# Optimization experiments

Measured on AMD Instinct MI355X. Metric: run time of the kernel, lower is better.

The kernel has to match this reference:

```python
import jax, jax.numpy as jnp
import numpy as np

BATCH, IN_F, OUT_F, GRID_PLUS_ORDER = 8192, 1024, 1024, 8

def setup_inputs() -> dict:
    key = jax.random.key(0)
    k1, k2, k3 = jax.random.split(key, 3)
    x = jax.random.normal(k1, (BATCH, IN_F), dtype=jnp.float32)
    base_weight = jax.random.normal(k2, (OUT_F, IN_F), dtype=jnp.float32) * 0.03
    spline_weight = jax.random.normal(k3, (OUT_F, IN_F, GRID_PLUS_ORDER), dtype=jnp.float32) * 0.1
    return {"x": x, "base_weight": base_weight, "spline_weight": spline_weight}

def reference(x, base_weight, spline_weight):
    # base_output = F.linear(x, base_weight) -> x @ W_b^T
    base_output = x @ base_weight.T  # [B, out]
    # Original: sum_{i,g} silu(x)[b,i] * spline_weight[o,i,g]
    # The grid/order axis g is never contracted with x, so it collapses:
    # silu(x) @ spline_weight.sum(-1).T  -- identical math, no [O,B,I,G] blowup.
    w_spline = jnp.sum(spline_weight, axis=-1)  # [out, in]
    spline_output = jax.nn.silu(x) @ w_spline.T  # [B, out]
    return base_output + spline_output
```

## Files before the change

kernel.cpp:

```cpp
#include <hip/hip_runtime.h>
#include <hip/hip_bf16.h>


#define BATCH 8192
#define IN_F 1024
#define OUT_F 1024
#define KP 2048

typedef unsigned short ushort_t;
typedef __attribute__((ext_vector_type(8))) short short8;
typedef __attribute__((ext_vector_type(4))) float f32x4;

__device__ __forceinline__ ushort_t f2bf(float f) {
  union { float f; unsigned int u; } v;
  v.f = f;
  unsigned int u = v.u;
  u += 0x7fffu + ((u >> 16) & 1u);
  return (ushort_t)(u >> 16);
}

#define PREP_A_BLOCKS 4096
#define PREP_S_BLOCKS 1024
#define PREP_B_BLOCKS 1024
#define PREP_BLOCKS (PREP_A_BLOCKS + PREP_S_BLOCKS + PREP_B_BLOCKS)

__global__ __launch_bounds__(256) void prep_all(
    const float* __restrict__ x, const float* __restrict__ Wb,
    const float* __restrict__ Ws, ushort_t* __restrict__ Apack,
    ushort_t* __restrict__ Wpack) {
  const int blk = blockIdx.x;
  const int t = threadIdx.x;

  if (blk < PREP_A_BLOCKS) {
    const int idx = blk * 256 + t;
    const int b = idx >> 7;
    const int i = (idx & 127) << 3;
    const float4 x0 = *(const float4*)(x + ((size_t)b << 10) + i);
    const float4 x1 = *(const float4*)(x + ((size_t)b << 10) + i + 4);
    float xv[8] = {x0.x, x0.y, x0.z, x0.w, x1.x, x1.y, x1.z, x1.w};
    ushort_t vb[8], vs[8];
#pragma unroll
    for (int j = 0; j < 8; ++j) {
      vb[j] = f2bf(xv[j]);
      vs[j] = f2bf(xv[j] / (1.0f + __expf(-xv[j])));
    }
    ushort_t* row = Apack + ((size_t)b << 11);
    *(short8*)(row + i) = *(short8*)vb;
    *(short8*)(row + IN_F + i) = *(short8*)vs;
  } else if (blk < PREP_A_BLOCKS + PREP_S_BLOCKS) {
    const int idx = (blk - PREP_A_BLOCKS) * 256 + t;
    const int o = idx >> 8;
    const int i0 = (idx & 255) << 2;
    ushort_t vs[4];
#pragma unroll
    for (int j = 0; j < 4; ++j) {
      const float4* p = (const float4*)(Ws + ((((size_t)o << 10) + i0 + j) << 3));
      const float4 a = p[0];
      const float4 b = p[1];
      vs[j] = f2bf(((a.x + a.y) + (a.z + a.w)) + ((b.x + b.y) + (b.z + b.w)));
    }
    *(ushort4*)(Wpack + ((size_t)o << 11) + IN_F + i0) = *(ushort4*)vs;
  } else {
    const int idx = (blk - PREP_A_BLOCKS - PREP_S_BLOCKS) * 256 + t;
    const int o = idx >> 8;
    const int c = (idx & 255) << 2;
    const float4 w = *(const float4*)(Wb + ((size_t)o << 10) + c);
    ushort4 v;
    v.x = f2bf(w.x); v.y = f2bf(w.y); v.z = f2bf(w.z); v.w = f2bf(w.w);
    *(ushort4*)(Wpack + ((size_t)o << 11) + c) = v;
  }
}

__global__ __launch_bounds__(256) void gemm_packed(
    const ushort_t* __restrict__ A,
    const ushort_t* __restrict__ W,
    float* __restrict__ C) {
  __shared__ ushort_t As[2 * 4096];
  __shared__ ushort_t Bs[2 * 4096];

  const int t = threadIdx.x;
  const int flat = blockIdx.y * 8 + blockIdx.x;
  const int xcd = flat & 7;
  const int local = flat >> 3;
  const int nt = local >> 3;
  const int mt = xcd * 8 + (local & 7);

  const int lane = t & 63;
  const int wave = t >> 6;
  const int wr = wave >> 1;
  const int wc = wave & 1;

  const int r = t >> 2;
  const int c = t & 3;
  const ushort_t* a_g = A + ((size_t)(mt * 128 + r)) * KP + c * 8;
  const ushort_t* b_g = W + ((size_t)(nt * 128 + r)) * KP + c * 8;
  const size_t rowskip = (size_t)64 * KP;
  const int wbase = c * 1024 + ((r ^ (c << 2)) << 3);

  f32x4 acc[4][4];
#pragma unroll
  for (int mi = 0; mi < 4; ++mi)
#pragma unroll
    for (int ni = 0; ni < 4; ++ni) acc[mi][ni] = (f32x4){0.f, 0.f, 0.f, 0.f};

  const int ks = lane >> 4;
  const int ar = (wr * 64 + (lane & 15)) ^ (ks << 2);
  const int br = (wc * 64 + (lane & 15)) ^ (ks << 2);
  const int rbase = ks * 1024;

  {
    uint4 la0 = *(const uint4*)(a_g);
    uint4 la1 = *(const uint4*)(a_g + rowskip);
    uint4 lb0 = *(const uint4*)(b_g);
    uint4 lb1 = *(const uint4*)(b_g + rowskip);
    *(uint4*)(As + wbase) = la0;
    *(uint4*)(As + wbase + 512) = la1;
    *(uint4*)(Bs + wbase) = lb0;
    *(uint4*)(Bs + wbase + 512) = lb1;
  }
  __syncthreads();

  int poff = 0;
  for (int k0 = 0; k0 < KP; k0 += 32) {
    const bool more = (k0 + 32) < KP;
    uint4 na0, na1, nb0, nb1;
    if (more) {
      na0 = *(const uint4*)(a_g + k0 + 32);
      na1 = *(const uint4*)(a_g + k0 + 32 + rowskip);
      nb0 = *(const uint4*)(b_g + k0 + 32);
      nb1 = *(const uint4*)(b_g + k0 + 32 + rowskip);
    }

    const ushort_t* ab = As + poff + rbase;
    const ushort_t* bb = Bs + poff + rbase;
    short8 af[4], bfr[4];
#pragma unroll
    for (int mi = 0; mi < 4; ++mi)
      af[mi] = *(const short8*)(ab + ((ar + mi * 16) << 3));
#pragma unroll
    for (int ni = 0; ni < 4; ++ni)
      bfr[ni] = *(const short8*)(bb + ((br + ni * 16) << 3));

#pragma unroll
    for (int mi = 0; mi < 4; ++mi)
#pragma unroll
      for (int ni = 0; ni < 4; ++ni)
        acc[mi][ni] = __builtin_amdgcn_mfma_f32_16x16x32_bf16(af[mi], bfr[ni], acc[mi][ni], 0, 0, 0);

    if (more) {
      const int qoff = poff ^ 4096;
      *(uint4*)(As + qoff + wbase) = na0;
      *(uint4*)(As + qoff + wbase + 512) = na1;
      *(uint4*)(Bs + qoff + wbase) = nb0;
      *(uint4*)(Bs + qoff + wbase + 512) = nb1;
      __syncthreads();
    }
    poff ^= 4096;
  }

  const int col0 = nt * 128 + wc * 64 + (lane & 15);
  const int row0 = mt * 128 + wr * 64 + ((lane >> 4) << 2);
#pragma unroll
  for (int mi = 0; mi < 4; ++mi)
#pragma unroll
    for (int ni = 0; ni < 4; ++ni) {
      float* cp = C + (size_t)(row0 + mi * 16) * OUT_F + col0 + ni * 16;
#pragma unroll
      for (int rr = 0; rr < 4; ++rr) cp[(size_t)rr * OUT_F] = acc[mi][ni][rr];
    }
}

extern "C" void kernel_launch(void* const* d_in, const int* in_sizes, int n_in,
                              void* d_out, int out_size, void* d_ws, size_t ws_size,
                              hipStream_t stream) {
  const float* x = (const float*)d_in[0];
  const float* wb = (const float*)d_in[1];
  const float* ws = (const float*)d_in[2];
  float* out = (float*)d_out;

  ushort_t* Apack = (ushort_t*)d_ws;
  ushort_t* Wpack = (ushort_t*)((char*)d_ws + (size_t)BATCH * KP * 2);

  prep_all<<<PREP_BLOCKS, 256, 0, stream>>>(x, wb, ws, Apack, Wpack);
  gemm_packed<<<dim3(OUT_F / 128, BATCH / 128), 256, 0, stream>>>(Apack, Wpack, out);
}
```

Measured before the change: 153.7 us.

## Restructure GEMM with 256x128 tiles, async global-to-LDS loads, triple buffering

Result: faster. 143.6 us (-6.5%).

```diff
diff --git a/kernel.cpp b/kernel.cpp
--- a/kernel.cpp
+++ b/kernel.cpp
@@ -71,31 +71,92 @@
   }
 }
 
-__global__ __launch_bounds__(256) void gemm_packed(
+#define BM 256
+#define BN 128
+#define GBK 64
+#define NSTEP (KP / GBK)
+#define A_US 16384
+#define B_US 8192
+#define BUF_US (A_US + B_US)
+#define NBUF 3
+
+typedef const __attribute__((address_space(1))) unsigned int gas_uint;
+typedef __attribute__((address_space(3))) unsigned int las_uint;
+#define ASYNC16(l, g) \
+  __builtin_amdgcn_global_load_lds((gas_uint*)(g), (las_uint*)(l), 16, 0, 0)
+
+__device__ __forceinline__ void stage_tile(const ushort_t* ga, const ushort_t* gb,
+                                           ushort_t* la, ushort_t* lb,
+                                           size_t rskip) {
+  ASYNC16(la, ga);
+  ASYNC16(la + 4096, ga + rskip);
+  ASYNC16(la + 8192, ga + 2 * rskip);
+  ASYNC16(la + 12288, ga + 3 * rskip);
+  ASYNC16(lb, gb);
+  ASYNC16(lb + 4096, gb + rskip);
+}
+
+__device__ __forceinline__ void mfma_step(const ushort_t* __restrict__ ab,
+                                          const ushort_t* __restrict__ bb,
+                                          const int (&aoff)[2][4],
+                                          const int (&boff)[2][4],
+                                          f32x4 (&acc)[4][4]) {
+#pragma unroll
+  for (int kk = 0; kk < 2; ++kk) {
+    short8 af[4], bf[4];
+#pragma unroll
+    for (int i = 0; i < 4; ++i) af[i] = *(const short8*)(ab + aoff[kk][i]);
+#pragma unroll
+    for (int i = 0; i < 4; ++i) bf[i] = *(const short8*)(bb + boff[kk][i]);
+    __builtin_amdgcn_s_setprio(1);
+#pragma unroll
+    for (int mi = 0; mi < 4; ++mi)
+#pragma unroll
+      for (int ni = 0; ni < 4; ++ni)
+        acc[mi][ni] = __builtin_amdgcn_mfma_f32_16x16x32_bf16(
+            af[mi], bf[ni], acc[mi][ni], 0, 0, 0);
+    __builtin_amdgcn_s_setprio(0);
+  }
+}
+
+__global__ __launch_bounds__(512, 2) void gemm_packed(
     const ushort_t* __restrict__ A,
     const ushort_t* __restrict__ W,
     float* __restrict__ C) {
-  __shared__ ushort_t As[2 * 4096];
-  __shared__ ushort_t Bs[2 * 4096];
+  __shared__ __align__(16) ushort_t lds[NBUF * BUF_US];
 
   const int t = threadIdx.x;
-  const int flat = blockIdx.y * 8 + blockIdx.x;
+  const int flat = blockIdx.x;
   const int xcd = flat & 7;
   const int local = flat >> 3;
-  const int nt = local >> 3;
-  const int mt = xcd * 8 + (local & 7);
+  const int nt = local >> 2;
+  const int mt = xcd * 4 + (local & 3);
 
   const int lane = t & 63;
   const int wave = t >> 6;
   const int wr = wave >> 1;
   const int wc = wave & 1;
-
-  const int r = t >> 2;
-  const int c = t & 3;
-  const ushort_t* a_g = A + ((size_t)(mt * 128 + r)) * KP + c * 8;
-  const ushort_t* b_g = W + ((size_t)(nt * 128 + r)) * KP + c * 8;
-  const size_t rowskip = (size_t)64 * KP;
-  const int wbase = c * 1024 + ((r ^ (c << 2)) << 3);
+  const int lr = lane & 15;
+  const int lq = lane >> 4;
+
+  const int srow = t >> 3;
+  const int kc = (t & 7) ^ (srow & 7);
+  const ushort_t* ga = A + (size_t)(mt * BM + srow) * KP + kc * 8;
+  const ushort_t* gb = W + (size_t)(nt * BN + srow) * KP + kc * 8;
+  const int ldst = t * 8;
+  const size_t rskip = (size_t)64 * KP;
+
+  int aoff[2][4], boff[2][4];
+#pragma unroll
+  for (int kk = 0; kk < 2; ++kk)
+#pragma unroll
+    for (int i = 0; i < 4; ++i) {
+      const int arow = wr * 64 + i * 16 + lr;
+      const int brow = wc * 64 + i * 16 + lr;
+      const int ks = kk * 4 + lq;
+      aoff[kk][i] = arow * 64 + ((ks ^ (arow & 7)) << 3);
+      boff[kk][i] = brow * 64 + ((ks ^ (brow & 7)) << 3);
+    }
 
   f32x4 acc[4][4];
 #pragma unroll
@@ -103,63 +164,38 @@
 #pragma unroll
     for (int ni = 0; ni < 4; ++ni) acc[mi][ni] = (f32x4){0.f, 0.f, 0.f, 0.f};
 
-  const int ks = lane >> 4;
-  const int ar = (wr * 64 + (lane & 15)) ^ (ks << 2);
-  const int br = (wc * 64 + (lane & 15)) ^ (ks << 2);
-  const int rbase = ks * 1024;
-
-  {
-    uint4 la0 = *(const uint4*)(a_g);
-    uint4 la1 = *(const uint4*)(a_g + rowskip);
-    uint4 lb0 = *(const uint4*)(b_g);
-    uint4 lb1 = *(const uint4*)(b_g + rowskip);
-    *(uint4*)(As + wbase) = la0;
-    *(uint4*)(As + wbase + 512) = la1;
-    *(uint4*)(Bs + wbase) = lb0;
-    *(uint4*)(Bs + wbase + 512) = lb1;
+  stage_tile(ga, gb, lds + ldst, lds + A_US + ldst, rskip);
+  stage_tile(ga + GBK, gb + GBK, lds + BUF_US + ldst, lds + BUF_US + A_US + ldst,
+             rskip);
+  asm volatile("s_waitcnt vmcnt(6)" ::: "memory");
+  __builtin_amdgcn_s_barrier();
+  __builtin_amdgcn_sched_barrier(0);
+
+  int co = 0;
+  int so = 2 * BUF_US;
+  const ushort_t* gpa = ga + 2 * GBK;
+  const ushort_t* gpb = gb + 2 * GBK;
+#pragma unroll 3
+  for (int s = 0; s < NSTEP - 2; ++s) {
+    stage_tile(gpa, gpb, lds + so + ldst, lds + so + A_US + ldst, rskip);
+    gpa += GBK;
+    gpb += GBK;
+    mfma_step(lds + co, lds + co + A_US, aoff, boff, acc);
+    asm volatile("s_waitcnt vmcnt(6)" ::: "memory");
+    __builtin_amdgcn_s_barrier();
+    __builtin_amdgcn_sched_barrier(0);
+    co += BUF_US; if (co == NBUF * BUF_US) co = 0;
+    so += BUF_US; if (so == NBUF * BUF_US) so = 0;
   }
-  __syncthreads();
-
-  int poff = 0;
-  for (int k0 = 0; k0 < KP; k0 += 32) {
-    const bool more = (k0 + 32) < KP;
-    uint4 na0, na1, nb0, nb1;
-    if (more) {
-      na0 = *(const uint4*)(a_g + k0 + 32);
-      na1 = *(const uint4*)(a_g + k0 + 32 + rowskip);
-      nb0 = *(const uint4*)(b_g + k0 + 32);
-      nb1 = *(const uint4*)(b_g + k0 + 32 + rowskip);
-    }
-
-    const ushort_t* ab = As + poff + rbase;
-    const ushort_t* bb = Bs + poff + rbase;
-    short8 af[4], bfr[4];
-#pragma unroll
-    for (int mi = 0; mi < 4; ++mi)
-      af[mi] = *(const short8*)(ab + ((ar + mi * 16) << 3));
-#pragma unroll
-    for (int ni = 0; ni < 4; ++ni)
-      bfr[ni] = *(const short8*)(bb + ((br + ni * 16) << 3));
-
-#pragma unroll
-    for (int mi = 0; mi < 4; ++mi)
-#pragma unroll
-      for (int ni = 0; ni < 4; ++ni)
-        acc[mi][ni] = __builtin_amdgcn_mfma_f32_16x16x32_bf16(af[mi], bfr[ni], acc[mi][ni], 0, 0, 0);
-
-    if (more) {
-      const int qoff = poff ^ 4096;
-      *(uint4*)(As + qoff + wbase) = na0;
-      *(uint4*)(As + qoff + wbase + 512) = na1;
-      *(uint4*)(Bs + qoff + wbase) = nb0;
-      *(uint4*)(Bs + qoff + wbase + 512) = nb1;
-      __syncthreads();
-    }
-    poff ^= 4096;
-  }
-
-  const int col0 = nt * 128 + wc * 64 + (lane & 15);
-  const int row0 = mt * 128 + wr * 64 + ((lane >> 4) << 2);
+  mfma_step(lds + co, lds + co + A_US, aoff, boff, acc);
+  asm volatile("s_waitcnt vmcnt(0)" ::: "memory");
+  __builtin_amdgcn_s_barrier();
+  __builtin_amdgcn_sched_barrier(0);
+  co += BUF_US; if (co == NBUF * BUF_US) co = 0;
+  mfma_step(lds + co, lds + co + A_US, aoff, boff, acc);
+
+  const int col0 = nt * BN + wc * 64 + lr;
+  const int row0 = mt * BM + wr * 64 + (lq << 2);
 #pragma unroll
   for (int mi = 0; mi < 4; ++mi)
 #pragma unroll
@@ -182,5 +218,5 @@
   ushort_t* Wpack = (ushort_t*)((char*)d_ws + (size_t)BATCH * KP * 2);
 
   prep_all<<<PREP_BLOCKS, 256, 0, stream>>>(x, wb, ws, Apack, Wpack);
-  gemm_packed<<<dim3(OUT_F / 128, BATCH / 128), 256, 0, stream>>>(Apack, Wpack, out);
-}
+  gemm_packed<<<dim3((BATCH / BM) * (OUT_F / BN)), dim3(512), 0, stream>>>(Apack, Wpack, out);
+}
```
